# Optimization experiments

Hardware: AMD Instinct MI355X
Metric: run time of the kernel (lower is better)

Reference implementation:

```python
import jax, jax.numpy as jnp
import numpy as np

K = 40        # knn neighbors (hard-coded in forward)
BN_EPS = 1e-5
NEG_SLOPE = 0.2
NHEADS = 8
ADIM = 64
HDIM = NHEADS * ADIM  # 512
SCALE = HDIM ** (-0.5)  # note: original scales by hdim**-0.5, not adim**-0.5


def knn_idx(x, k):
    # x: (B, C, N) -> (B, N, k) indices of k nearest neighbors (incl. self)
    xx = jnp.sum(x * x, axis=1)                       # (B, N)
    inner = jnp.einsum('bcn,bcm->bnm', x, x)          # (B, N, N)
    neg_sq_dist = 2.0 * inner - xx[:, :, None] - xx[:, None, :]
    return jax.lax.top_k(neg_sq_dist, k)[1]           # (B, N, k)


def get_graph_feature(x, k):
    # x: (B, C, N) -> (B, 2C, N, k)
    idx = knn_idx(x, k)                               # (B, N, k) int32
    xt = jnp.transpose(x, (0, 2, 1))                  # (B, N, C)
    feat = jax.vmap(lambda pts, ids: pts[ids])(xt, idx)  # (B, N, k, C)
    center = xt[:, :, None, :]                        # (B, N, 1, C)
    out = jnp.concatenate(
        [feat - center, jnp.broadcast_to(center, feat.shape)], axis=-1)
    return jnp.transpose(out, (0, 3, 1, 2))           # (B, 2C, N, k)


def bn_lrelu(h, g, b, m, v):
    # inference-mode BatchNorm2d over channel axis=1 + LeakyReLU(0.2)
    scale = g / jnp.sqrt(v + BN_EPS)
    h = (h - m[None, :, None, None]) * scale[None, :, None, None] + b[None, :, None, None]
    return jax.nn.leaky_relu(h, NEG_SLOPE)


def branch(p, conv5_w, bn5_g, bn5_b, bn5_m, bn5_v, conv6_w, bn6_g, bn6_b, bn6_m, bn6_v):
    g = get_graph_feature(p, K)                       # (B, 1024, N, k)
    h = jnp.einsum('oc,bcnk->bonk', conv5_w, g)       # (B, 512, N, k)
    h = bn_lrelu(h, bn5_g, bn5_b, bn5_m, bn5_v)
    h = jnp.transpose(h, (0, 2, 1, 3))                # (B, N=2048, 512, k)
    h = jnp.einsum('oc,bcnk->bonk', conv6_w, h)       # (B, 515, 512, k)
    h = bn_lrelu(h, bn6_g, bn6_b, bn6_m, bn6_v)
    h = jnp.transpose(h, (0, 2, 1, 3))                # (B, 512, 515, k)
    return jnp.max(h, axis=-1)                        # (B, 512, 515)


def heads(f, W):
    # f: (B, S, indim), W: (hdim, indim) -> (B, nheads, S, adim)
    q = jnp.einsum('bsi,oi->bso', f, W)
    B, S, _ = q.shape
    return jnp.transpose(q.reshape(B, S, NHEADS, ADIM), (0, 2, 1, 3))


def setup_inputs() -> dict:
    key = jax.random.key(0)
    ks = jax.random.split(key, 8)
    B, C, N = 1, 512, 2048
    indim = 515
    inp = {
        'x': jax.random.normal(ks[0], (B, C, N), jnp.float32),
        'y': jax.random.normal(ks[1], (B, C, N), jnp.float32),
        'conv5_w': jax.random.normal(ks[2], (512, 1024), jnp.float32) * 0.02,
        'bn5_g': jnp.ones((512,), jnp.float32),
        'bn5_b': jnp.zeros((512,), jnp.float32),
        'bn5_m': jnp.zeros((512,), jnp.float32),
        'bn5_v': jnp.ones((512,), jnp.float32),
        'conv6_w': jax.random.normal(ks[3], (515, 2048), jnp.float32) * 0.02,
        'bn6_g': jnp.ones((515,), jnp.float32),
        'bn6_b': jnp.zeros((515,), jnp.float32),
        'bn6_m': jnp.zeros((515,), jnp.float32),
        'bn6_v': jnp.ones((515,), jnp.float32),
        'Wq': jax.random.normal(ks[4], (HDIM, indim), jnp.float32) * 0.02,
        'Wk': jax.random.normal(ks[5], (HDIM, indim), jnp.float32) * 0.02,
        'Wv': jax.random.normal(ks[6], (HDIM, indim), jnp.float32) * 0.02,
        'Wout': jax.random.normal(ks[7], (indim, HDIM), jnp.float32) * 0.02,
        'bout': jnp.zeros((indim,), jnp.float32),
    }
    return inp


def reference(x, y, conv5_w, bn5_g, bn5_b, bn5_m, bn5_v,
              conv6_w, bn6_g, bn6_b, bn6_m, bn6_v,
              Wq, Wk, Wv, Wout, bout):
    xf = branch(x, conv5_w, bn5_g, bn5_b, bn5_m, bn5_v,
                conv6_w, bn6_g, bn6_b, bn6_m, bn6_v)   # (B, 512, 515)
    yf = branch(y, conv5_w, bn5_g, bn5_b, bn5_m, bn5_v,
                conv6_w, bn6_g, bn6_b, bn6_m, bn6_v)   # (B, 512, 515)
    q = heads(xf, Wq)                                  # (B, H, 512, adim)
    k = heads(yf, Wk)
    v = heads(yf, Wv)
    scores = jax.nn.softmax(jnp.einsum('bhsd,bhtd->bhst', q, k) * SCALE, axis=-1)
    weighted = jnp.einsum('bhst,bhtd->bhsd', scores, v)  # (B, H, 512, adim)
    B, H, S, D = weighted.shape
    merged = jnp.transpose(weighted, (0, 2, 1, 3)).reshape(B, S, H * D)
    return jnp.einsum('bsh,oh->bso', merged, Wout) + bout  # (B, 512, 515)
```

## Files before the change

kernel.cpp:

```cpp
#include <hip/hip_runtime.h>
#include <hip/hip_bf16.h>

typedef __bf16 bf16_t;
typedef float f32x4 __attribute__((ext_vector_type(4)));
typedef __bf16 bf16x8 __attribute__((ext_vector_type(8)));

#define ASYNC_COPY16(gptr, lptr) \
    __builtin_amdgcn_global_load_lds((const __attribute__((address_space(1))) void*)(gptr), \
                                     (__attribute__((address_space(3))) void*)(lptr), 16, 0, 0)

__device__ __forceinline__ float ldx(const void* p, long i, int isbf) {
    return isbf ? (float)((const bf16_t*)p)[i] : ((const float*)p)[i];
}

__global__ __launch_bounds__(256)
void detect_dtype(const void* __restrict__ x, int n, int* __restrict__ flags)
{
    __shared__ int red[4];
    const int tid = threadIdx.x;
    const int ns = n < 8192 ? n : 8192;
    int cnt = 0;
    for (int i = tid; i < ns; i += 256) {
        float v = (float)((const bf16_t*)x)[i];
        float a = fabsf(v);
        bool pl = (v == 0.f) || (a >= 6e-8f && a <= 1.7e7f);
        cnt += pl ? 1 : 0;
    }
    for (int o = 32; o; o >>= 1) cnt += __shfl_down(cnt, o);
    if ((tid & 63) == 0) red[tid >> 6] = cnt;
    __syncthreads();
    if (tid == 0) {
        int t = red[0] + red[1] + red[2] + red[3];
        flags[0] = (t * 10 >= ns * 9) ? 1 : 0;
    }
}

struct C3 { const void* p[3]; bf16_t* d[3]; int n[3]; };
__global__ __launch_bounds__(256)
void conv_elem3(C3 c, const int* __restrict__ flag)
{
    const int isbf = *flag;
    const int z = blockIdx.z, n = c.n[z];
    bf16_t* dst = c.d[z];
    const void* src = c.p[z];
    for (long i = blockIdx.x * 256L + threadIdx.x; i < n; i += (long)gridDim.x * 256)
        dst[i] = (bf16_t)ldx(src, i, isbf);
}

struct P9 { const void* p[9]; int n[9]; };
__global__ __launch_bounds__(256)
void conv_param(P9 pk, float* __restrict__ dst, const int* __restrict__ flag)
{
    const int isbf = *flag;
    const int b = blockIdx.x, n = pk.n[b];
    for (int j = threadIdx.x; j < n; j += 256)
        dst[b * 544 + j] = ldx(pk.p[b], j, isbf);
}

struct P3 { const void* p[3]; };
__global__ __launch_bounds__(256)
void pad_wf3(P3 ps, bf16_t* __restrict__ Wp0, const int* __restrict__ flag)
{
    const int isbf = *flag;
    const int z = blockIdx.z;
    const long i = blockIdx.x * 256L + threadIdx.x;
    if (i >= 512 * 544) return;
    const long o = i / 544, c = i % 544;
    bf16_t* Wp = Wp0 + (size_t)z * 512 * 544;
    Wp[i] = (c < 515) ? (bf16_t)ldx(ps.p[z], o * 515 + c, isbf) : (bf16_t)0.f;
}

__global__ __launch_bounds__(256)
void transpose_split(const void* __restrict__ X, bf16_t* __restrict__ XtA,
                     bf16_t* __restrict__ XtB, const int* __restrict__ flag)
{
    __shared__ __align__(16) bf16_t thi[32][33];
    __shared__ __align__(16) bf16_t tlo[32][33];
    const int isbf = *flag;
    const int n0 = blockIdx.x * 32, c0 = blockIdx.y * 32;
    const int lx = threadIdx.x & 31, ly = threadIdx.x >> 5;
    for (int i = 0; i < 4; ++i) {
        float v = ldx(X, (long)(c0 + ly + i * 8) * 2048 + n0 + lx, isbf);
        bf16_t hi = (bf16_t)v;
        thi[ly + i * 8][lx] = hi;
        tlo[ly + i * 8][lx] = (bf16_t)(v - (float)hi);
    }
    __syncthreads();
    for (int i = 0; i < 4; ++i) {
        const long n = n0 + ly + i * 8;
        const int c = c0 + lx;
        bf16_t hi = thi[lx][ly + i * 8], lo = tlo[lx][ly + i * 8];
        XtA[n * 1536 + c] = hi;  XtA[n * 1536 + 512 + c] = lo;  XtA[n * 1536 + 1024 + c] = hi;
        XtB[n * 1536 + c] = hi;  XtB[n * 1536 + 512 + c] = hi;  XtB[n * 1536 + 1024 + c] = lo;
    }
}

__global__ __launch_bounds__(256)
void xx_kernel(const bf16_t* __restrict__ XtA, float* __restrict__ xx)
{
    const long n = blockIdx.x * 256L + threadIdx.x;
    float acc = 0.f;
    for (int c = 0; c < 512; ++c) {
        float v = (float)XtA[n * 1536 + c] + (float)XtA[n * 1536 + 512 + c];
        acc += v * v;
    }
    xx[n] = acc;
}

__global__ __launch_bounds__(256)
void gemm128d(const bf16_t* __restrict__ A, const bf16_t* __restrict__ B,
              float* __restrict__ C, int M, int N, int K, int lda, int ldb, int ldc)
{
    __shared__ __align__(16) bf16_t As[2][4096];
    __shared__ __align__(16) bf16_t Bs[2][4096];
    const int tid = threadIdx.x;
    int mt, nt;
    if ((gridDim.y & 7) == 0) {
        const int bid = blockIdx.y * gridDim.x + blockIdx.x;
        const int xcd = bid & 7, s = bid >> 3;
        mt = s % gridDim.x;
        nt = xcd + 8 * (s / gridDim.x);
    } else { mt = blockIdx.x; nt = blockIdx.y; }
    const int m0 = mt * 128, n0 = nt * 128;
    const int wave = tid >> 6, lane = tid & 63;
    const int wm = (wave >> 1) * 64, wn = (wave & 1) * 64;
    const int l15 = lane & 15, quad = lane >> 4;

    const bf16_t* ga[2]; const bf16_t* gb[2]; int loff[2];
    for (int i = 0; i < 2; ++i) {
        const int q = wave * 2 + i;
        const int seg = q & 3, half = q >> 2;
        const int row = half * 64 + lane;
        long ar = min((long)(m0 + row), (long)M - 1);
        long br = min((long)(n0 + row), (long)N - 1);
        ga[i] = A + ar * lda + seg * 8;
        gb[i] = B + br * ldb + seg * 8;
        loff[i] = seg * 1024 + half * 512;
    }

    f32x4 acc[4][4] = {};

    for (int i = 0; i < 2; ++i) {
        ASYNC_COPY16(ga[i], &As[0][loff[i]]);
        ASYNC_COPY16(gb[i], &Bs[0][loff[i]]);
    }

    for (int k0 = 0; k0 < K; k0 += 32) {
        const int cur = (k0 >> 5) & 1;
        __syncthreads();
        if (k0 + 32 < K) {
            for (int i = 0; i < 2; ++i) {
                ASYNC_COPY16(ga[i] + k0 + 32, &As[cur ^ 1][loff[i]]);
                ASYNC_COPY16(gb[i] + k0 + 32, &Bs[cur ^ 1][loff[i]]);
            }
        }
        bf16x8 af[4], bfr[4];
        for (int mi = 0; mi < 4; ++mi)
            af[mi] = *(const bf16x8*)&As[cur][quad * 1024 + (wm + mi * 16 + l15) * 8];
        for (int ni = 0; ni < 4; ++ni)
            bfr[ni] = *(const bf16x8*)&Bs[cur][quad * 1024 + (wn + ni * 16 + l15) * 8];
        for (int mi = 0; mi < 4; ++mi)
        for (int ni = 0; ni < 4; ++ni)
            acc[mi][ni] = __builtin_amdgcn_mfma_f32_16x16x32_bf16(af[mi], bfr[ni], acc[mi][ni], 0, 0, 0);
    }

    for (int mi = 0; mi < 4; ++mi)
    for (int ni = 0; ni < 4; ++ni)
    for (int r = 0; r < 4; ++r) {
        int gm = m0 + wm + mi * 16 + quad * 4 + r;
        int gn = n0 + wn + ni * 16 + l15;
        if (gm >= M || gn >= N) continue;
        C[(long)gm * ldc + gn] = acc[mi][ni][r];
    }
}

__global__ __launch_bounds__(256)
void epi6_max(const float* __restrict__ C2c, const float* __restrict__ p6,
              bf16_t* __restrict__ Fb, int c0, int Nc)
{
    const int cl = blockIdx.x, tid = threadIdx.x;
    for (int o2 = tid; o2 < 544; o2 += 256) {
        float r = 0.f;
        if (o2 < 515) {
            const float sc = p6[o2] / sqrtf(p6[3 * 544 + o2] + 1e-5f);
            const float mu = p6[2 * 544 + o2], bb = p6[1 * 544 + o2];
            const float4* p = (const float4*)(C2c + (long)o2 * Nc + cl * 40);
            float mx = -__builtin_inff();
            for (int k4 = 0; k4 < 10; ++k4) {
                float4 v = p[k4];
                float hv[4] = {v.x, v.y, v.z, v.w};
                for (int j = 0; j < 4; ++j) {
                    float h = (hv[j] - mu) * sc + bb;
                    h = h >= 0.f ? h : 0.2f * h;
                    mx = fmaxf(mx, h);
                }
            }
            r = mx;
        }
        Fb[(long)(c0 + cl) * 544 + o2] = (bf16_t)r;
    }
}

__global__ __launch_bounds__(256)
void gemm64d(const bf16_t* __restrict__ A, const bf16_t* __restrict__ B,
             float* __restrict__ C, const float* __restrict__ xx,
             int M, int N, int K, int lda, int ldb, int ldc,
             long aBS, long bBS, long cBS, int epi, int moff)
{
    __shared__ __align__(16) bf16_t As[2][4 * 64 * 8];
    __shared__ __align__(16) bf16_t Bs[2][4 * 64 * 8];
    const int tid = threadIdx.x;
    const int m0 = blockIdx.y * 64, n0 = blockIdx.x * 64;
    if (epi == 4 && n0 < m0) return;
    const int bz = blockIdx.z;
    A += (long)bz * aBS;
    B += (long)bz * bBS;
    const int wave = tid >> 6, lane = tid & 63;
    const int wm = (wave >> 1) * 32, wn = (wave & 1) * 32;
    const int l15 = lane & 15, quad = lane >> 4;

    const long ar = min((long)(m0 + lane), (long)M - 1);
    const long br = min((long)(n0 + lane), (long)N - 1);
    const bf16_t* ga = A + ar * lda + wave * 8;
    const bf16_t* gb = B + br * ldb + wave * 8;

    f32x4 acc[2][2] = {};

    ASYNC_COPY16(ga, &As[0][wave * 512]);
    ASYNC_COPY16(gb, &Bs[0][wave * 512]);

    for (int k0 = 0; k0 < K; k0 += 32) {
        const int cur = (k0 >> 5) & 1;
        __syncthreads();
        if (k0 + 32 < K) {
            ASYNC_COPY16(ga + k0 + 32, &As[cur ^ 1][wave * 512]);
            ASYNC_COPY16(gb + k0 + 32, &Bs[cur ^ 1][wave * 512]);
        }
        bf16x8 af0 = *(const bf16x8*)&As[cur][quad * 512 + (wm +      l15) * 8];
        bf16x8 af1 = *(const bf16x8*)&As[cur][quad * 512 + (wm + 16 + l15) * 8];
        bf16x8 bf0 = *(const bf16x8*)&Bs[cur][quad * 512 + (wn +      l15) * 8];
        bf16x8 bf1 = *(const bf16x8*)&Bs[cur][quad * 512 + (wn + 16 + l15) * 8];
        acc[0][0] = __builtin_amdgcn_mfma_f32_16x16x32_bf16(af0, bf0, acc[0][0], 0, 0, 0);
        acc[0][1] = __builtin_amdgcn_mfma_f32_16x16x32_bf16(af0, bf1, acc[0][1], 0, 0, 0);
        acc[1][0] = __builtin_amdgcn_mfma_f32_16x16x32_bf16(af1, bf0, acc[1][0], 0, 0, 0);
        acc[1][1] = __builtin_amdgcn_mfma_f32_16x16x32_bf16(af1, bf1, acc[1][1], 0, 0, 0);
    }

    C += (long)bz * cBS;
    for (int mi = 0; mi < 2; ++mi)
    for (int ni = 0; ni < 2; ++ni)
    for (int r = 0; r < 4; ++r) {
        int gm = m0 + wm + mi * 16 + quad * 4 + r;
        int gn = n0 + wn + ni * 16 + l15;
        if (gm >= M || gn >= N) continue;
        float o = acc[mi][ni][r];
        if (epi == 4) {
            float v = 2.f * o - xx[gm] - xx[gn];
            C[(long)gm * ldc + gn] = v;
            C[(long)gn * ldc + gm] = v;
        } else if (epi == 1) {
            C[(long)gm * ldc + gn] = 2.f * o - xx[gm + moff] - xx[gn];
        } else {
            C[(long)gm * ldc + gn] = o;
        }
    }
}

__global__ __launch_bounds__(256)
void gemm_nt(const bf16_t* __restrict__ A, const bf16_t* __restrict__ B,
             void* __restrict__ Cv, const float* __restrict__ bias,
             const int* __restrict__ oflag, float alpha,
             int M, int N, int K, int lda, int ldb, int ldc,
             long aBS, long bBS, long cBS, int epi)
{
    __shared__ __align__(16) bf16_t As[64 * 40];
    __shared__ __align__(16) bf16_t Bs[64 * 40];
    const int tid = threadIdx.x;
    const int m0 = blockIdx.y * 64, n0 = blockIdx.x * 64;
    const int bz = blockIdx.z;
    A += (long)bz * aBS;
    B += (long)bz * bBS;

    const int lrow = tid >> 2;
    const int lseg = (tid & 3) * 8;
    const long arow = min(m0 + lrow, M - 1);
    const long brow = min(n0 + lrow, N - 1);
    const bf16_t* ap = A + arow * lda + lseg;
    const bf16_t* bp = B + brow * ldb + lseg;

    const int wave = tid >> 6, lane = tid & 63;
    const int wm = (wave >> 1) * 32, wn = (wave & 1) * 32;
    const int l15 = lane & 15, quad = lane >> 4;

    f32x4 acc[2][2] = {};

    for (int k0 = 0; k0 < K; k0 += 32) {
        int4 av = *(const int4*)ap;  ap += 32;
        int4 bv = *(const int4*)bp;  bp += 32;
        __syncthreads();
        *(int4*)(&As[lrow * 40 + lseg]) = av;
        *(int4*)(&Bs[lrow * 40 + lseg]) = bv;
        __syncthreads();
        bf16x8 af0 = *(const bf16x8*)(&As[(wm +      l15) * 40 + quad * 8]);
        bf16x8 af1 = *(const bf16x8*)(&As[(wm + 16 + l15) * 40 + quad * 8]);
        bf16x8 bf0 = *(const bf16x8*)(&Bs[(wn +      l15) * 40 + quad * 8]);
        bf16x8 bf1 = *(const bf16x8*)(&Bs[(wn + 16 + l15) * 40 + quad * 8]);
        acc[0][0] = __builtin_amdgcn_mfma_f32_16x16x32_bf16(af0, bf0, acc[0][0], 0, 0, 0);
        acc[0][1] = __builtin_amdgcn_mfma_f32_16x16x32_bf16(af0, bf1, acc[0][1], 0, 0, 0);
        acc[1][0] = __builtin_amdgcn_mfma_f32_16x16x32_bf16(af1, bf0, acc[1][0], 0, 0, 0);
        acc[1][1] = __builtin_amdgcn_mfma_f32_16x16x32_bf16(af1, bf1, acc[1][1], 0, 0, 0);
    }

    const int ofl = oflag ? *oflag : 1;
    for (int mi = 0; mi < 2; ++mi)
    for (int ni = 0; ni < 2; ++ni)
    for (int r = 0; r < 4; ++r) {
        int gm = m0 + wm + mi * 16 + quad * 4 + r;
        int gn = n0 + wn + ni * 16 + l15;
        if (gm >= M || gn >= N) continue;
        float o = acc[mi][ni][r];
        long cidx = (long)bz * cBS + (long)gm * ldc + gn;
        switch (epi) {
        case 2: ((bf16_t*)Cv)[cidx] = (bf16_t)o; break;
        case 3: ((float*)Cv)[cidx] = o * alpha; break;
        case 5: ((bf16_t*)Cv)[(long)bz * cBS + (long)gn * ldc + gm] = (bf16_t)o; break;
        case 6: {
            float w = o + bias[gn];
            if (ofl) ((bf16_t*)Cv)[cidx] = (bf16_t)w;
            else     ((float*)Cv)[cidx]  = w;
        } break;
        }
    }
}

__global__ __launch_bounds__(256)
void topk40_bs(const float* __restrict__ S, int* __restrict__ idx_out)
{
    __shared__ int red[4];
    __shared__ unsigned long long tmask[8][4];
    __shared__ int sh_slot;
    __shared__ unsigned cu[48];
    __shared__ int      ci[48];
    const int row = blockIdx.x, tid = threadIdx.x;
    const int wave = tid >> 6, lane = tid & 63;

    unsigned uvr[8];
    for (int c = 0; c < 8; ++c) {
        unsigned x = __float_as_uint(S[(long)row * 2048 + c * 256 + tid]);
        uvr[c] = (x & 0x80000000u) ? ~x : (x | 0x80000000u);
    }
    if (tid == 0) sh_slot = 0;

    unsigned lo = 0u, hi = 0xFFFFFFFFu;
    while (hi - lo > 1u) {
        unsigned mid = lo + ((hi - lo) >> 1);
        int c = 0;
        for (int i = 0; i < 8; ++i) c += (uvr[i] > mid) ? 1 : 0;
        for (int o = 32; o; o >>= 1) c += __shfl_down(c, o);
        if (lane == 0) red[wave] = c;
        __syncthreads();
        int tot = red[0] + red[1] + red[2] + red[3];
        __syncthreads();
        if (tot >= 40) lo = mid; else hi = mid;
    }
    const unsigned thr = hi;

    for (int c = 0; c < 8; ++c)
        if (uvr[c] > thr) {
            int s = atomicAdd(&sh_slot, 1);
            cu[s] = uvr[c]; ci[s] = c * 256 + tid;
        }
    for (int c = 0; c < 8; ++c) {
        unsigned long long m = __ballot(uvr[c] == thr);
        if (lane == 0) tmask[c][wave] = m;
    }
    __syncthreads();
    const int want = 40 - sh_slot;
    int base = 0;
    for (int c = 0; c < 8; ++c) {
        if (uvr[c] == thr) {
            int r = base;
            for (int w = 0; w < wave; ++w) r += __popcll(tmask[c][w]);
            r += __popcll(tmask[c][wave] & (((unsigned long long)1 << lane) - 1));
            if (r < want) {
                int s = atomicAdd(&sh_slot, 1);
                cu[s] = uvr[c]; ci[s] = c * 256 + tid;
            }
        }
        for (int w = 0; w < 4; ++w) base += __popcll(tmask[c][w]);
    }
    __syncthreads();
    if (tid < 40) {
        unsigned u = cu[tid]; int i = ci[tid];
        int r = 0;
        for (int j = 0; j < 40; ++j)
            r += (cu[j] > u || (cu[j] == u && ci[j] < i)) ? 1 : 0;
        idx_out[row * 40 + r] = i;
    }
}

__global__ __launch_bounds__(256)
void h1a_gen(const float* __restrict__ T, const float* __restrict__ U,
             const int* __restrict__ idx, const float* __restrict__ pf,
             bf16_t* __restrict__ Hc, int c0)
{
    __shared__ int idxs[40 * 256];
    const int c5 = c0 + blockIdx.y, n0 = blockIdx.x * 256, tid = threadIdx.x;
    for (int i = tid; i < 40 * 256; i += 256)
        idxs[(i % 40) * 256 + (i / 40)] = idx[n0 * 40 + i] & 2047;
    const float sc = pf[c5] / sqrtf(pf[3 * 544 + c5] + 1e-5f);
    const float mu = pf[2 * 544 + c5], bb = pf[1 * 544 + c5];
    const float q  = U[(long)c5 * 2048 + n0 + tid] - T[(long)c5 * 2048 + n0 + tid];
    const float* Trow = T + (long)c5 * 2048;
    __syncthreads();
    for (int k = 0; k < 40; ++k) {
        float h = Trow[idxs[k * 256 + tid]] + q;
        h = (h - mu) * sc + bb;
        h = h >= 0.f ? h : 0.2f * h;
        Hc[(long)(blockIdx.y * 40 + k) * 2048 + n0 + tid] = (bf16_t)h;
    }
}

__global__ __launch_bounds__(256)
void softmax_row(const float* __restrict__ Sc, bf16_t* __restrict__ P)
{
    __shared__ float red[4];
    const long r = blockIdx.x;
    const int tid = threadIdx.x, lane = tid & 63, wave = tid >> 6;
    const float* row = Sc + r * 512;
    float v0 = row[tid], v1 = row[tid + 256];
    float mx = fmaxf(v0, v1);
    for (int off = 32; off; off >>= 1) mx = fmaxf(mx, __shfl_down(mx, off));
    if (lane == 0) red[wave] = mx;
    __syncthreads();
    mx = fmaxf(fmaxf(red[0], red[1]), fmaxf(red[2], red[3]));
    __syncthreads();
    float e0 = expf(v0 - mx), e1 = expf(v1 - mx);
    float sm = e0 + e1;
    for (int off = 32; off; off >>= 1) sm += __shfl_down(sm, off);
    if (lane == 0) red[wave] = sm;
    __syncthreads();
    sm = red[0] + red[1] + red[2] + red[3];
    float inv = 1.f / sm;
    P[r * 512 + tid] = (bf16_t)(e0 * inv);
    P[r * 512 + tid + 256] = (bf16_t)(e1 * inv);
}

extern "C" void kernel_launch(void* const* d_in, const int* in_sizes, int n_in,
                              void* d_out, int out_size, void* d_ws, size_t ws_size,
                              hipStream_t stream)
{
    (void)n_in; (void)out_size;

    char* wsb = (char*)d_ws;
    size_t pos = 0;
    auto alloc = [&](size_t bytes) -> char* {
        char* p = wsb + pos;
        pos += (bytes + 255) & ~(size_t)255;
        return p;
    };
    int*    flags = (int*)  alloc(256);
    int*    idx   = (int*)  alloc(2048 * 40 * 4);
    float*  xx    = (float*)alloc(2048 * 4);
    float*  T     = (float*)alloc((size_t)512 * 2048 * 4);
    float*  U     = (float*)alloc((size_t)512 * 2048 * 4);
    bf16_t* XtA   = (bf16_t*)alloc((size_t)2048 * 1536 * 2);
    bf16_t* XtB   = (bf16_t*)alloc((size_t)2048 * 1536 * 2);
    bf16_t* W5c   = (bf16_t*)alloc((size_t)512 * 1024 * 2);
    bf16_t* W6c   = (bf16_t*)alloc((size_t)515 * 2048 * 2);
    bf16_t* Woutc = (bf16_t*)alloc((size_t)515 * 512 * 2);
    bf16_t* Wqp   = (bf16_t*)alloc((size_t)512 * 544 * 2);
    bf16_t* Wkp   = (bf16_t*)alloc((size_t)512 * 544 * 2);
    bf16_t* Wvp   = (bf16_t*)alloc((size_t)512 * 544 * 2);
    float*  pf    = (float*)alloc((size_t)9 * 544 * 4);
    bf16_t* Fb[2];
    Fb[0] = (bf16_t*)alloc((size_t)512 * 544 * 2);
    Fb[1] = (bf16_t*)alloc((size_t)512 * 544 * 2);
    bf16_t* qb = (bf16_t*)alloc((size_t)512 * 512 * 2);
    bf16_t* kb = (bf16_t*)alloc((size_t)512 * 512 * 2);
    bf16_t* vt = (bf16_t*)alloc((size_t)512 * 512 * 2);
    bf16_t* mg = (bf16_t*)alloc((size_t)512 * 512 * 2);
    char* BIG = wsb + pos;
    size_t big = (ws_size > pos) ? (ws_size - pos) : 0;
    if (big < 3939840) return;

    const int CC = (big >= 126074880) ? 512 : (big >= 63037440) ? 256
                 : (big >= 31518720)  ? 128 : (big >= 15759360) ? 64
                 : (big >= 7879680)   ? 32  : 16;
    const int RC = (big >= 16777216) ? 2048 : (big >= 4194304) ? 512 : 128;
    const int AH = (big >= 12582912) ? 8 : 1;
    const int Nc = CC * 40;

    float*  S   = (float*)BIG;
    bf16_t* Hc  = (bf16_t*)BIG;
    float*  C2c = (float*)(BIG + (size_t)Nc * 2048 * 2);
    float*  scA = (float*)BIG;
    bf16_t* prA = (bf16_t*)(BIG + (size_t)AH * 512 * 512 * 4);

    detect_dtype<<<1, 256, 0, stream>>>(d_in[0], in_sizes[0], flags);
    C3 c3;
    c3.p[0] = d_in[2];  c3.d[0] = W5c;   c3.n[0] = 512 * 1024;
    c3.p[1] = d_in[7];  c3.d[1] = W6c;   c3.n[1] = 515 * 2048;
    c3.p[2] = d_in[15]; c3.d[2] = Woutc; c3.n[2] = 515 * 512;
    conv_elem3<<<dim3(512, 1, 3), 256, 0, stream>>>(c3, flags);
    P3 p3;
    p3.p[0] = d_in[12]; p3.p[1] = d_in[13]; p3.p[2] = d_in[14];
    pad_wf3<<<dim3(1088, 1, 3), 256, 0, stream>>>(p3, Wqp, flags);
    P9 pk;
    const int pidx[9] = {3, 4, 5, 6, 8, 9, 10, 11, 16};
    for (int i = 0; i < 9; ++i) { pk.p[i] = d_in[pidx[i]]; pk.n[i] = in_sizes[pidx[i]]; }
    conv_param<<<9, 256, 0, stream>>>(pk, pf, flags);

    for (int b = 0; b < 2; ++b) {
        transpose_split<<<dim3(64, 16), 256, 0, stream>>>(d_in[b], XtA, XtB, flags);
        xx_kernel<<<8, 256, 0, stream>>>(XtA, xx);
        if (RC == 2048) {
            gemm64d<<<dim3(32, 32), 256, 0, stream>>>(XtA, XtB, S,
                xx, 2048, 2048, 1536, 1536, 1536, 2048, 0, 0, 0, 4, 0);
            topk40_bs<<<2048, 256, 0, stream>>>(S, idx);
        } else {
            for (int r0 = 0; r0 < 2048; r0 += RC) {
                gemm64d<<<dim3(32, RC / 64), 256, 0, stream>>>(XtA + (size_t)r0 * 1536, XtB, S,
                    xx, RC, 2048, 1536, 1536, 1536, 2048, 0, 0, 0, 1, r0);
                topk40_bs<<<RC, 256, 0, stream>>>(S, idx + (size_t)r0 * 40);
            }
        }
        gemm64d<<<dim3(32, 8, 2), 256, 0, stream>>>(W5c, XtA, T, nullptr,
            512, 2048, 512, 1024, 1536, 2048, 512, 0, (long)512 * 2048, 0, 0);
        for (int c0 = 0; c0 < 512; c0 += CC) {
            h1a_gen<<<dim3(8, CC), 256, 0, stream>>>(T, U, idx, pf, Hc, c0);
            gemm128d<<<dim3(5, Nc / 128), 256, 0, stream>>>(W6c, Hc, C2c,
                515, Nc, 2048, 2048, 2048, Nc);
            epi6_max<<<CC, 256, 0, stream>>>(C2c, pf + 4 * 544, Fb[b], c0, Nc);
        }
    }

    gemm_nt<<<dim3(8, 8, 2), 256, 0, stream>>>(Fb[0], Wqp, qb, nullptr, nullptr, 0.f,
        512, 512, 544, 544, 544, 512,
        (long)512 * 544, (long)512 * 544, (long)512 * 512, 2);
    gemm_nt<<<dim3(8, 8, 1), 256, 0, stream>>>(Fb[1], Wvp, vt, nullptr, nullptr, 0.f,
        512, 512, 544, 544, 544, 512, 0, 0, 0, 5);

    const float SCALE = 0.04419417382415922f;
    if (AH == 8) {
        gemm_nt<<<dim3(8, 8, 8), 256, 0, stream>>>(qb, kb, scA, nullptr, nullptr, SCALE,
            512, 512, 64, 512, 512, 512, 64, 64, 262144, 3);
        softmax_row<<<4096, 256, 0, stream>>>(scA, prA);
        gemm_nt<<<dim3(1, 8, 8), 256, 0, stream>>>(prA, vt, mg, nullptr, nullptr, 0.f,
            512, 64, 512, 512, 512, 512, 262144, 32768, 64, 2);
    } else {
        for (int h = 0; h < 8; ++h) {
            gemm_nt<<<dim3(8, 8, 1), 256, 0, stream>>>(qb + h * 64, kb + h * 64, scA,
                nullptr, nullptr, SCALE, 512, 512, 64, 512, 512, 512, 0, 0, 0, 3);
            softmax_row<<<512, 256, 0, stream>>>(scA, prA);
            gemm_nt<<<dim3(1, 8, 1), 256, 0, stream>>>(prA, vt + (size_t)h * 64 * 512,
                mg + h * 64, nullptr, nullptr, 0.f,
                512, 64, 512, 512, 512, 512, 0, 0, 0, 2);
        }
    }
    gemm_nt<<<dim3(9, 8, 1), 256, 0, stream>>>(mg, Woutc, d_out, pf + 8 * 544, flags,
        0.f, 512, 515, 512, 512, 512, 515, 0, 0, 0, 6);
}
```

Before: 875.3 us.

## Load GEMM fragments directly from global memory into registers, bypassing LDS

The 128x128 conv6 GEMM no longer stages A/B tiles through double-buffered shared memory with async copies and barriers. Each lane now loads its MFMA fragments straight from global memory into registers, software-pipelined two k-steps deep. This removes the LDS traffic and __syncthreads, but it drops reuse of tiles across waves, so each wave re-reads rows that other waves share. That raises L2/global load volume and exposes more latency per wave.

New measurement: 970.6 us. 1.11x slower.

```diff
diff --git a/kernel.cpp b/kernel.cpp
--- a/kernel.cpp
+++ b/kernel.cpp
@@ -108,11 +108,9 @@
 }
 
 __global__ __launch_bounds__(256)
-void gemm128d(const bf16_t* __restrict__ A, const bf16_t* __restrict__ B,
+void gemm128r(const bf16_t* __restrict__ A, const bf16_t* __restrict__ B,
               float* __restrict__ C, int M, int N, int K, int lda, int ldb, int ldc)
 {
-    __shared__ __align__(16) bf16_t As[2][4096];
-    __shared__ __align__(16) bf16_t Bs[2][4096];
     const int tid = threadIdx.x;
     int mt, nt;
     if ((gridDim.y & 7) == 0) {
@@ -126,42 +124,39 @@
     const int wm = (wave >> 1) * 64, wn = (wave & 1) * 64;
     const int l15 = lane & 15, quad = lane >> 4;
 
-    const bf16_t* ga[2]; const bf16_t* gb[2]; int loff[2];
-    for (int i = 0; i < 2; ++i) {
-        const int q = wave * 2 + i;
-        const int seg = q & 3, half = q >> 2;
-        const int row = half * 64 + lane;
-        long ar = min((long)(m0 + row), (long)M - 1);
-        long br = min((long)(n0 + row), (long)N - 1);
-        ga[i] = A + ar * lda + seg * 8;
-        gb[i] = B + br * ldb + seg * 8;
-        loff[i] = seg * 1024 + half * 512;
+    const bf16_t* ap[4];
+    const bf16_t* bp[4];
+    for (int mi = 0; mi < 4; ++mi) {
+        long r = min((long)(m0 + wm + mi * 16 + l15), (long)M - 1);
+        ap[mi] = A + r * lda + quad * 8;
+    }
+    for (int ni = 0; ni < 4; ++ni) {
+        long r = min((long)(n0 + wn + ni * 16 + l15), (long)N - 1);
+        bp[ni] = B + r * ldb + quad * 8;
     }
 
     f32x4 acc[4][4] = {};
-
-    for (int i = 0; i < 2; ++i) {
-        ASYNC_COPY16(ga[i], &As[0][loff[i]]);
-        ASYNC_COPY16(gb[i], &Bs[0][loff[i]]);
-    }
-
-    for (int k0 = 0; k0 < K; k0 += 32) {
-        const int cur = (k0 >> 5) & 1;
-        __syncthreads();
-        if (k0 + 32 < K) {
-            for (int i = 0; i < 2; ++i) {
-                ASYNC_COPY16(ga[i] + k0 + 32, &As[cur ^ 1][loff[i]]);
-                ASYNC_COPY16(gb[i] + k0 + 32, &Bs[cur ^ 1][loff[i]]);
-            }
-        }
-        bf16x8 af[4], bfr[4];
-        for (int mi = 0; mi < 4; ++mi)
-            af[mi] = *(const bf16x8*)&As[cur][quad * 1024 + (wm + mi * 16 + l15) * 8];
-        for (int ni = 0; ni < 4; ++ni)
-            bfr[ni] = *(const bf16x8*)&Bs[cur][quad * 1024 + (wn + ni * 16 + l15) * 8];
+    bf16x8 a0[4], b0[4], a1[4], b1[4];
+
+    for (int i = 0; i < 4; ++i) { a0[i] = *(const bf16x8*)(ap[i]); b0[i] = *(const bf16x8*)(bp[i]); }
+
+    for (int k0 = 0; k0 < K; k0 += 64) {
+        for (int i = 0; i < 4; ++i) {
+            a1[i] = *(const bf16x8*)(ap[i] + k0 + 32);
+            b1[i] = *(const bf16x8*)(bp[i] + k0 + 32);
+        }
         for (int mi = 0; mi < 4; ++mi)
         for (int ni = 0; ni < 4; ++ni)
-            acc[mi][ni] = __builtin_amdgcn_mfma_f32_16x16x32_bf16(af[mi], bfr[ni], acc[mi][ni], 0, 0, 0);
+            acc[mi][ni] = __builtin_amdgcn_mfma_f32_16x16x32_bf16(a0[mi], b0[ni], acc[mi][ni], 0, 0, 0);
+        if (k0 + 64 < K) {
+            for (int i = 0; i < 4; ++i) {
+                a0[i] = *(const bf16x8*)(ap[i] + k0 + 64);
+                b0[i] = *(const bf16x8*)(bp[i] + k0 + 64);
+            }
+        }
+        for (int mi = 0; mi < 4; ++mi)
+        for (int ni = 0; ni < 4; ++ni)
+            acc[mi][ni] = __builtin_amdgcn_mfma_f32_16x16x32_bf16(a1[mi], b1[ni], acc[mi][ni], 0, 0, 0);
     }
 
     for (int mi = 0; mi < 4; ++mi)
@@ -529,7 +524,7 @@
             512, 2048, 512, 1024, 1536, 2048, 512, 0, (long)512 * 2048, 0, 0);
         for (int c0 = 0; c0 < 512; c0 += CC) {
             h1a_gen<<<dim3(8, CC), 256, 0, stream>>>(T, U, idx, pf, Hc, c0);
-            gemm128d<<<dim3(5, Nc / 128), 256, 0, stream>>>(W6c, Hc, C2c,
+            gemm128r<<<dim3(5, Nc / 128), 256, 0, stream>>>(W6c, Hc, C2c,
                 515, Nc, 2048, 2048, 2048, Nc);
             epi6_max<<<CC, 256, 0, stream>>>(C2c, pf + 4 * 544, Fb[b], c0, Nc);
         }
```

## Fold conv6 tail rows into last M-tile and store GEMM output as bf16

Applied to the files above, without the earlier changes.

The conv6 GEMM (M=515) previously used a fifth M-tile that computed only 3 useful rows. Now the grid has four M-tiles, and the tile with mt==3 also loads a 16-row strip (rows 512-527) and has two of its waves compute it with extra MFMAs. The intermediate C2 buffer is also stored as bf16 instead of fp32, which halves its write and read traffic and lets larger chunk sizes fit the workspace. The costs are added work and imbalance on one M-tile, and lower precision before the BN and max epilogue. The XCD swizzle is now applied unconditionally.

Result: no change. 872.2 us (-0.4%).

```diff
diff --git a/kernel.cpp b/kernel.cpp
--- a/kernel.cpp
+++ b/kernel.cpp
@@ -4,6 +4,7 @@
 typedef __bf16 bf16_t;
 typedef float f32x4 __attribute__((ext_vector_type(4)));
 typedef __bf16 bf16x8 __attribute__((ext_vector_type(8)));
+typedef __bf16 bf16x4 __attribute__((ext_vector_type(4)));
 
 #define ASYNC_COPY16(gptr, lptr) \
     __builtin_amdgcn_global_load_lds((const __attribute__((address_space(1))) void*)(gptr), \
@@ -109,22 +110,24 @@
 
 __global__ __launch_bounds__(256)
 void gemm128d(const bf16_t* __restrict__ A, const bf16_t* __restrict__ B,
-              float* __restrict__ C, int M, int N, int K, int lda, int ldb, int ldc)
+              bf16_t* __restrict__ C, int M, int N, int K, int lda, int ldb, int ldc)
 {
     __shared__ __align__(16) bf16_t As[2][4096];
     __shared__ __align__(16) bf16_t Bs[2][4096];
+    __shared__ __align__(16) bf16_t As2[2][512];
     const int tid = threadIdx.x;
     int mt, nt;
-    if ((gridDim.y & 7) == 0) {
+    {
         const int bid = blockIdx.y * gridDim.x + blockIdx.x;
         const int xcd = bid & 7, s = bid >> 3;
         mt = s % gridDim.x;
         nt = xcd + 8 * (s / gridDim.x);
-    } else { mt = blockIdx.x; nt = blockIdx.y; }
+    }
     const int m0 = mt * 128, n0 = nt * 128;
     const int wave = tid >> 6, lane = tid & 63;
     const int wm = (wave >> 1) * 64, wn = (wave & 1) * 64;
     const int l15 = lane & 15, quad = lane >> 4;
+    const bool xrows = (mt == 3);
 
     const bf16_t* ga[2]; const bf16_t* gb[2]; int loff[2];
     for (int i = 0; i < 2; ++i) {
@@ -137,13 +140,20 @@
         gb[i] = B + br * ldb + seg * 8;
         loff[i] = seg * 1024 + half * 512;
     }
+    const bf16_t* ga2 = nullptr;
+    if (xrows) {
+        long r2 = min((long)(512 + (lane & 15)), (long)M - 1);
+        ga2 = A + r2 * lda + (lane >> 4) * 8;
+    }
 
     f32x4 acc[4][4] = {};
+    f32x4 acc4[4] = {};
 
     for (int i = 0; i < 2; ++i) {
         ASYNC_COPY16(ga[i], &As[0][loff[i]]);
         ASYNC_COPY16(gb[i], &Bs[0][loff[i]]);
     }
+    if (xrows && wave == 0) ASYNC_COPY16(ga2, &As2[0][0]);
 
     for (int k0 = 0; k0 < K; k0 += 32) {
         const int cur = (k0 >> 5) & 1;
@@ -153,6 +163,7 @@
                 ASYNC_COPY16(ga[i] + k0 + 32, &As[cur ^ 1][loff[i]]);
                 ASYNC_COPY16(gb[i] + k0 + 32, &Bs[cur ^ 1][loff[i]]);
             }
+            if (xrows && wave == 0) ASYNC_COPY16(ga2 + k0 + 32, &As2[cur ^ 1][0]);
         }
         bf16x8 af[4], bfr[4];
         for (int mi = 0; mi < 4; ++mi)
@@ -162,6 +173,11 @@
         for (int mi = 0; mi < 4; ++mi)
         for (int ni = 0; ni < 4; ++ni)
             acc[mi][ni] = __builtin_amdgcn_mfma_f32_16x16x32_bf16(af[mi], bfr[ni], acc[mi][ni], 0, 0, 0);
+        if (xrows && wm == 64) {
+            bf16x8 af4 = *(const bf16x8*)&As2[cur][(quad * 16 + l15) * 8];
+            for (int ni = 0; ni < 4; ++ni)
+                acc4[ni] = __builtin_amdgcn_mfma_f32_16x16x32_bf16(af4, bfr[ni], acc4[ni], 0, 0, 0);
+        }
     }
 
     for (int mi = 0; mi < 4; ++mi)
@@ -170,12 +186,21 @@
         int gm = m0 + wm + mi * 16 + quad * 4 + r;
         int gn = n0 + wn + ni * 16 + l15;
         if (gm >= M || gn >= N) continue;
-        C[(long)gm * ldc + gn] = acc[mi][ni][r];
-    }
-}
-
-__global__ __launch_bounds__(256)
-void epi6_max(const float* __restrict__ C2c, const float* __restrict__ p6,
+        C[(long)gm * ldc + gn] = (bf16_t)acc[mi][ni][r];
+    }
+    if (xrows && wm == 64) {
+        for (int ni = 0; ni < 4; ++ni)
+        for (int r = 0; r < 4; ++r) {
+            int gm = 512 + quad * 4 + r;
+            int gn = n0 + wn + ni * 16 + l15;
+            if (gm >= M || gn >= N) continue;
+            C[(long)gm * ldc + gn] = (bf16_t)acc4[ni][r];
+        }
+    }
+}
+
+__global__ __launch_bounds__(256)
+void epi6_max(const bf16_t* __restrict__ C2b, const float* __restrict__ p6,
               bf16_t* __restrict__ Fb, int c0, int Nc)
 {
     const int cl = blockIdx.x, tid = threadIdx.x;
@@ -184,13 +209,12 @@
         if (o2 < 515) {
             const float sc = p6[o2] / sqrtf(p6[3 * 544 + o2] + 1e-5f);
             const float mu = p6[2 * 544 + o2], bb = p6[1 * 544 + o2];
-            const float4* p = (const float4*)(C2c + (long)o2 * Nc + cl * 40);
+            const bf16x4* p = (const bf16x4*)(C2b + (long)o2 * Nc + cl * 40);
             float mx = -__builtin_inff();
             for (int k4 = 0; k4 < 10; ++k4) {
-                float4 v = p[k4];
-                float hv[4] = {v.x, v.y, v.z, v.w};
+                bf16x4 v = p[k4];
                 for (int j = 0; j < 4; ++j) {
-                    float h = (hv[j] - mu) * sc + bb;
+                    float h = ((float)v[j] - mu) * sc + bb;
                     h = h >= 0.f ? h : 0.2f * h;
                     mx = fmaxf(mx, h);
                 }
@@ -484,16 +508,16 @@
     size_t big = (ws_size > pos) ? (ws_size - pos) : 0;
     if (big < 3939840) return;
 
-    const int CC = (big >= 126074880) ? 512 : (big >= 63037440) ? 256
-                 : (big >= 31518720)  ? 128 : (big >= 15759360) ? 64
-                 : (big >= 7879680)   ? 32  : 16;
+    const int CC = (big >= 105000000) ? 512 : (big >= 52500000) ? 256
+                 : (big >= 26250000)  ? 128 : (big >= 13130000) ? 64
+                 : (big >= 6570000)   ? 32  : 16;
     const int RC = (big >= 16777216) ? 2048 : (big >= 4194304) ? 512 : 128;
     const int AH = (big >= 12582912) ? 8 : 1;
     const int Nc = CC * 40;
 
     float*  S   = (float*)BIG;
     bf16_t* Hc  = (bf16_t*)BIG;
-    float*  C2c = (float*)(BIG + (size_t)Nc * 2048 * 2);
+    bf16_t* C2b = (bf16_t*)(BIG + (size_t)Nc * 2048 * 2);
     float*  scA = (float*)BIG;
     bf16_t* prA = (bf16_t*)(BIG + (size_t)AH * 512 * 512 * 4);
 
@@ -529,9 +553,9 @@
             512, 2048, 512, 1024, 1536, 2048, 512, 0, (long)512 * 2048, 0, 0);
         for (int c0 = 0; c0 < 512; c0 += CC) {
             h1a_gen<<<dim3(8, CC), 256, 0, stream>>>(T, U, idx, pf, Hc, c0);
-            gemm128d<<<dim3(5, Nc / 128), 256, 0, stream>>>(W6c, Hc, C2c,
+            gemm128d<<<dim3(4, Nc / 128), 256, 0, stream>>>(W6c, Hc, C2b,
                 515, Nc, 2048, 2048, 2048, Nc);
-            epi6_max<<<CC, 256, 0, stream>>>(C2c, pf + 4 * 544, Fb[b], c0, Nc);
+            epi6_max<<<CC, 256, 0, stream>>>(C2b, pf + 4 * 544, Fb[b], c0, Nc);
         }
     }
 
```
